# Kernel optimization log

Hardware: AMD Instinct MI355X
Metric: run time of the kernel (lower is better)

Reference implementation:

```python
import jax, jax.numpy as jnp
import numpy as np

COMMITMENT_COST = 0.25

def setup_inputs() -> dict:
    key = jax.random.key(0)
    k1, k2 = jax.random.split(key)
    B, K, D = 32768, 4096, 256
    inputs = jax.random.normal(k1, (B, D), dtype=jnp.float32)
    embedding = jax.random.normal(k2, (K, D), dtype=jnp.float32) * (1.0 / np.sqrt(D))
    return {"inputs": inputs, "embedding": embedding}

def reference(inputs, embedding):
    distances = (
        jnp.sum(inputs * inputs, axis=1, keepdims=True)
        + jnp.sum(embedding * embedding, axis=1)
        - 2.0 * jnp.einsum("bd,kd->bk", inputs, embedding)
    )
    encoding_indices = jnp.argmin(distances, axis=1)  # [B]
    # one-hot @ embedding == gather
    quantized = embedding[encoding_indices]  # [B, D]
    # Eval-mode loss (module in inference mode): q_latent + commitment * e_latent
    e_latent_loss = jnp.mean((inputs - jax.lax.stop_gradient(quantized)) ** 2)
    q_latent_loss = jnp.mean((quantized - jax.lax.stop_gradient(inputs)) ** 2)
    loss = q_latent_loss + COMMITMENT_COST * e_latent_loss
    # Straight-through estimator
    quantized_st = inputs + jax.lax.stop_gradient(quantized - inputs)
    return (quantized_st, loss, encoding_indices)
```

## Files before the change

kernel.cpp:

```cpp
#include <hip/hip_runtime.h>

constexpr int Bsz = 32768;
constexpr int Ksz = 4096;
constexpr int Dsz = 256;

constexpr int KD = 512;
constexpr int NT = 12;
constexpr int NCAND = 16;
constexpr int NFBLK = Bsz / 4;
constexpr float TAU = 1e-3f;

typedef __attribute__((ext_vector_type(8))) short short8;
typedef __attribute__((ext_vector_type(4))) float f32x4;

__device__ __forceinline__ unsigned short f2bf(float f) {
  unsigned u = __float_as_uint(f);
  u += 0x7fffu + ((u >> 16) & 1u);
  return (unsigned short)(u >> 16);
}
__device__ __forceinline__ float bf2f(unsigned short h) {
  return __uint_as_float(((unsigned)h) << 16);
}

__global__ __launch_bounds__(256) void vq_prep_x(const float* __restrict__ X,
                                                 unsigned short* __restrict__ X2) {
  const int tid = blockIdx.x * 256 + threadIdx.x;
  const int row = tid >> 6;
  const int d4 = tid & 63;
  const float4 v = *reinterpret_cast<const float4*>(X + (size_t)row * Dsz + d4 * 4);
  ushort4 h, l;
  h.x = f2bf(v.x); l.x = f2bf(v.x - bf2f(h.x));
  h.y = f2bf(v.y); l.y = f2bf(v.y - bf2f(h.y));
  h.z = f2bf(v.z); l.z = f2bf(v.z - bf2f(h.z));
  h.w = f2bf(v.w); l.w = f2bf(v.w - bf2f(h.w));
  *reinterpret_cast<ushort4*>(X2 + (size_t)row * KD + d4 * 4) = h;
  *reinterpret_cast<ushort4*>(X2 + (size_t)row * KD + 256 + d4 * 4) = l;
}

__global__ __launch_bounds__(256) void vq_prep_e(const float* __restrict__ E,
                                                 unsigned short* __restrict__ E2,
                                                 float* __restrict__ enorm) {
  const int wid = threadIdx.x >> 6;
  const int lane = threadIdx.x & 63;
  const int k = blockIdx.x * 4 + wid;
  const float4 v = *reinterpret_cast<const float4*>(E + (size_t)k * Dsz + lane * 4);
  ushort4 h, l;
  h.x = f2bf(v.x); l.x = f2bf(v.x - bf2f(h.x));
  h.y = f2bf(v.y); l.y = f2bf(v.y - bf2f(h.y));
  h.z = f2bf(v.z); l.z = f2bf(v.z - bf2f(h.z));
  h.w = f2bf(v.w); l.w = f2bf(v.w - bf2f(h.w));
  *reinterpret_cast<ushort4*>(E2 + (size_t)k * KD + lane * 4) = h;
  *reinterpret_cast<ushort4*>(E2 + (size_t)k * KD + 256 + lane * 4) = l;
  float s = v.x * v.x + v.y * v.y + v.z * v.z + v.w * v.w;
#pragma unroll
  for (int off = 32; off > 0; off >>= 1) s += __shfl_down(s, off);
  if (lane == 0) enorm[k] = s;
}

__global__ __launch_bounds__(512, 2) void vq_gemm_argmin(
    const unsigned short* __restrict__ X2, const unsigned short* __restrict__ E2,
    const float* __restrict__ enorm, float4* __restrict__ cand) {
  __shared__ unsigned short sA[2][256 * 64];
  __shared__ unsigned short sB[2][256 * 64];

  const int t5 = threadIdx.x;
  const int lane = t5 & 63;
  const int wid = t5 >> 6;
  const int wm = wid >> 2;
  const int wn = wid & 3;

  const int bid = blockIdx.x;
  const int swz = (bid & 7) * 256 + (bid >> 3);
  const int mb = swz >> 4;
  const int nb = swz & 15;
  const int row0 = mb * 256;
  const int col0 = nb * 256;

  const int srow = lane >> 3;
  const int sslot = (lane & 7) ^ srow;

  const int l15 = lane & 15;
  const int lhi = lane >> 4;
  const int lx = lane & 7;

  f32x4 acc[8][4];
#pragma unroll
  for (int m = 0; m < 8; ++m)
#pragma unroll
    for (int n = 0; n < 4; ++n) acc[m][n] = f32x4{0.f, 0.f, 0.f, 0.f};

#define AOF(kt) ((((kt) >> 2) == 1 ? 256 : 0) + ((kt) & 3) * 64)
#define BOF(kt) ((((kt) >> 2) == 2 ? 256 : 0) + ((kt) & 3) * 64)

#define STAGE(BUFI, AO, BO)                                                    \
  {                                                                            \
    _Pragma("unroll") for (int q = 0; q < 4; ++q) {                            \
      const int r = wid * 32 + q * 8;                                          \
      __builtin_amdgcn_global_load_lds(                                        \
          (const __attribute__((address_space(1))) void*)(                     \
              X2 + (size_t)(row0 + r + srow) * KD + (AO) + sslot * 8),         \
          (__attribute__((address_space(3))) void*)(&sA[BUFI][r * 64]), 16, 0, 0); \
    }                                                                          \
    _Pragma("unroll") for (int q = 0; q < 4; ++q) {                            \
      const int r = wid * 32 + q * 8;                                          \
      __builtin_amdgcn_global_load_lds(                                        \
          (const __attribute__((address_space(1))) void*)(                     \
              E2 + (size_t)(col0 + r + srow) * KD + (BO) + sslot * 8),         \
          (__attribute__((address_space(3))) void*)(&sB[BUFI][r * 64]), 16, 0, 0); \
    }                                                                          \
  }

#define LOADFRAGS(BUFI, KS)                                                    \
  {                                                                            \
    _Pragma("unroll") for (int m = 0; m < 8; ++m)                              \
        af[m] = *reinterpret_cast<const short8*>(                              \
            &sA[BUFI][(wm * 128 + m * 16 + l15) * 64 +                         \
                      (((KS)*4 + lhi) ^ lx) * 8]);                             \
    _Pragma("unroll") for (int n = 0; n < 4; ++n)                              \
        bf[n] = *reinterpret_cast<const short8*>(                              \
            &sB[BUFI][(wn * 64 + n * 16 + l15) * 64 +                          \
                      (((KS)*4 + lhi) ^ lx) * 8]);                             \
  }

#define MFMAS                                                                  \
  {                                                                            \
    _Pragma("unroll") for (int m = 0; m < 8; ++m)                              \
        _Pragma("unroll") for (int n = 0; n < 4; ++n)                          \
            acc[m][n] = __builtin_amdgcn_mfma_f32_16x16x32_bf16(               \
                af[m], bf[n], acc[m][n], 0, 0, 0);                             \
  }

  STAGE(0, AOF(0), BOF(0));
  STAGE(1, AOF(1), BOF(1));

#pragma unroll
  for (int t = 0; t < NT; ++t) {
    const int buf = t & 1;
    short8 af[8], bf[4];

    if (t < NT - 1) {
      asm volatile("s_waitcnt vmcnt(8)" ::: "memory");
    } else {
      asm volatile("s_waitcnt vmcnt(0)" ::: "memory");
    }
    __builtin_amdgcn_sched_barrier(0);
    __builtin_amdgcn_s_barrier();
    __builtin_amdgcn_sched_barrier(0);

    LOADFRAGS(buf, 0);
    asm volatile("s_waitcnt lgkmcnt(0)" ::: "memory");
    __builtin_amdgcn_sched_barrier(0);
    __builtin_amdgcn_s_setprio(1);
    MFMAS;
    __builtin_amdgcn_s_setprio(0);

    LOADFRAGS(buf, 1);
    asm volatile("s_waitcnt lgkmcnt(0)" ::: "memory");
    __builtin_amdgcn_sched_barrier(0);
    __builtin_amdgcn_s_barrier();
    __builtin_amdgcn_sched_barrier(0);

    if (t + 2 < NT) {
      STAGE(buf, AOF(t + 2), BOF(t + 2));
    }
    __builtin_amdgcn_sched_barrier(0);

    __builtin_amdgcn_s_setprio(1);
    MFMAS;
    __builtin_amdgcn_s_setprio(0);
  }

  __syncthreads();

  float en[4];
#pragma unroll
  for (int n = 0; n < 4; ++n) en[n] = enorm[col0 + wn * 64 + n * 16 + l15];

  float4* scr = reinterpret_cast<float4*>(&sA[0][0]);

#pragma unroll
  for (int m = 0; m < 8; ++m) {
#pragma unroll
    for (int q = 0; q < 4; ++q) {
      float v1 = 3.4e38f, v2 = 3.4e38f;
      int ii1 = 0x7fffffff, ii2 = 0x7fffffff;
#pragma unroll
      for (int n = 0; n < 4; ++n) {
        const float s = en[n] - 2.0f * acc[m][n][q];
        const int colg = col0 + wn * 64 + n * 16 + l15;
        if (s < v1) { v2 = v1; ii2 = ii1; v1 = s; ii1 = colg; }
        else if (s < v2) { v2 = s; ii2 = colg; }
      }
#pragma unroll
      for (int mbit = 1; mbit <= 8; mbit <<= 1) {
        const float ov1 = __shfl_xor(v1, mbit);
        const float ov2 = __shfl_xor(v2, mbit);
        const int oi1 = __shfl_xor(ii1, mbit);
        const int oi2 = __shfl_xor(ii2, mbit);
        if (ov1 < v1 || (ov1 == v1 && oi1 < ii1)) {
          float nv2 = v1; int ni2 = ii1;
          if (ov2 < nv2) { nv2 = ov2; ni2 = oi2; }
          v1 = ov1; ii1 = oi1; v2 = nv2; ii2 = ni2;
        } else if (ov1 < v2) {
          v2 = ov1; ii2 = oi1;
        }
      }
      if (l15 == 0) {
        const int rl = wm * 128 + m * 16 + lhi * 4 + q;
        scr[rl * 4 + wn] = make_float4(v1, __int_as_float(ii1),
                                       v2, __int_as_float(ii2));
      }
    }
  }
  __syncthreads();
  if (t5 < 256) {
    float v1 = 3.4e38f, v2 = 3.4e38f;
    int ii1 = 0x7fffffff, ii2 = 0x7fffffff;
#pragma unroll
    for (int j = 0; j < 4; ++j) {
      const float4 c = scr[t5 * 4 + j];
      const float o1 = c.x, o2 = c.z;
      const int a1 = __float_as_int(c.y), a2 = __float_as_int(c.w);
      if (o1 < v1 || (o1 == v1 && a1 < ii1)) {
        float nv2 = v1; int ni2 = ii1;
        if (o2 < nv2) { nv2 = o2; ni2 = a2; }
        v2 = nv2; ii2 = ni2; v1 = o1; ii1 = a1;
      } else if (o1 < v2) {
        v2 = o1; ii2 = a1;
      }
    }
    cand[(size_t)(row0 + t5) * NCAND + nb] =
        make_float4(v1, __int_as_float(ii1), v2, __int_as_float(ii2));
  }
#undef AOF
#undef BOF
#undef STAGE
#undef LOADFRAGS
#undef MFMAS
}

__global__ __launch_bounds__(256) void vq_finalize(
    const float* __restrict__ X, const float* __restrict__ E,
    const float4* __restrict__ cand, float* __restrict__ out,
    float* __restrict__ partial) {
  __shared__ float ls[4];
  const int wid = threadIdx.x >> 6;
  const int lane = threadIdx.x & 63;
  const int b = blockIdx.x * 4 + wid;

  float v1 = 3.4e38f, v2 = 3.4e38f;
  int ii1 = 0x7fffffff, ii2 = 0x7fffffff;
  if (lane < NCAND) {
    const float4 c = cand[(size_t)b * NCAND + lane];
    v1 = c.x; ii1 = __float_as_int(c.y);
    v2 = c.z; ii2 = __float_as_int(c.w);
  }
#pragma unroll
  for (int mbit = 1; mbit <= 8; mbit <<= 1) {
    const float ov1 = __shfl_xor(v1, mbit);
    const float ov2 = __shfl_xor(v2, mbit);
    const int oi1 = __shfl_xor(ii1, mbit);
    const int oi2 = __shfl_xor(ii2, mbit);
    if (ov1 < v1 || (ov1 == v1 && oi1 < ii1)) {
      float nv2 = v1; int ni2 = ii1;
      if (ov2 < nv2) { nv2 = ov2; ni2 = oi2; }
      v1 = ov1; ii1 = oi1; v2 = nv2; ii2 = ni2;
    } else if (ov1 < v2) {
      v2 = ov1; ii2 = oi1;
    }
  }
  v1 = __shfl(v1, 0); v2 = __shfl(v2, 0);
  ii1 = __shfl(ii1, 0); ii2 = __shfl(ii2, 0);

  const float4 x = *reinterpret_cast<const float4*>(X + (size_t)b * Dsz + lane * 4);

  if (v2 - v1 < TAU) {
    const float4 e1 = *reinterpret_cast<const float4*>(E + (size_t)ii1 * Dsz + lane * 4);
    const float4 e2 = *reinterpret_cast<const float4*>(E + (size_t)ii2 * Dsz + lane * 4);
    double d1 = ((double)x.x - e1.x) * ((double)x.x - e1.x) +
                ((double)x.y - e1.y) * ((double)x.y - e1.y) +
                ((double)x.z - e1.z) * ((double)x.z - e1.z) +
                ((double)x.w - e1.w) * ((double)x.w - e1.w);
    double d2 = ((double)x.x - e2.x) * ((double)x.x - e2.x) +
                ((double)x.y - e2.y) * ((double)x.y - e2.y) +
                ((double)x.z - e2.z) * ((double)x.z - e2.z) +
                ((double)x.w - e2.w) * ((double)x.w - e2.w);
#pragma unroll
    for (int mbit = 1; mbit <= 32; mbit <<= 1) {
      d1 += __shfl_xor(d1, mbit);
      d2 += __shfl_xor(d2, mbit);
    }
    if (d2 < d1 || (d2 == d1 && ii2 < ii1)) ii1 = ii2;
  }

  const float4 q = *reinterpret_cast<const float4*>(E + (size_t)ii1 * Dsz + lane * 4);
  *reinterpret_cast<float4*>(out + (size_t)b * Dsz + lane * 4) = q;

  const float dx = x.x - q.x, dy = x.y - q.y, dz = x.z - q.z, dw = x.w - q.w;
  float s2 = dx * dx + dy * dy + dz * dz + dw * dw;
#pragma unroll
  for (int off = 32; off > 0; off >>= 1) s2 += __shfl_down(s2, off);
  if (lane == 0) {
    ls[wid] = s2;
    out[(size_t)Bsz * Dsz + 1 + b] = (float)ii1;
  }
  __syncthreads();
  if (threadIdx.x == 0)
    partial[blockIdx.x] = ls[0] + ls[1] + ls[2] + ls[3];
}

__global__ __launch_bounds__(256) void vq_loss_reduce(const float* __restrict__ partial,
                                                      float* __restrict__ out) {
  __shared__ float ls[4];
  const int wid = threadIdx.x >> 6;
  const int lane = threadIdx.x & 63;
  float s = 0.f;
  for (int i = threadIdx.x; i < NFBLK; i += 256) s += partial[i];
#pragma unroll
  for (int off = 32; off > 0; off >>= 1) s += __shfl_down(s, off);
  if (lane == 0) ls[wid] = s;
  __syncthreads();
  if (threadIdx.x == 0)
    out[(size_t)Bsz * Dsz] = (ls[0] + ls[1] + ls[2] + ls[3]) *
                             (1.25f / ((float)Bsz * (float)Dsz));
}

extern "C" void kernel_launch(void* const* d_in, const int* in_sizes, int n_in,
                              void* d_out, int out_size, void* d_ws, size_t ws_size,
                              hipStream_t stream) {
  const float* X = (const float*)d_in[0];
  const float* E = (const float*)d_in[1];
  float* out = (float*)d_out;

  char* ws = (char*)d_ws;
  float* enorm = (float*)ws;
  unsigned short* X2 = (unsigned short*)(ws + (16 << 10));
  unsigned short* E2 = (unsigned short*)(ws + (16 << 10) + (32 << 20));
  float4* cand = (float4*)(ws + (16 << 10) + (36 << 20));
  float* partial = (float*)(ws + (16 << 10) + (44 << 20));

  vq_prep_x<<<Bsz * 64 / 256, 256, 0, stream>>>(X, X2);
  vq_prep_e<<<Ksz / 4, 256, 0, stream>>>(E, E2, enorm);
  vq_gemm_argmin<<<(Bsz / 256) * (Ksz / 256), 512, 0, stream>>>(X2, E2, enorm, cand);
  vq_finalize<<<NFBLK, 256, 0, stream>>>(X, E, cand, out, partial);
  vq_loss_reduce<<<1, 256, 0, stream>>>(partial, out);
}
```

Measured before the change: 449.4 us.

## Split each K-tile into four quadrant MFMA phases with interleaved LDS fragment loads

Restructures the main GEMM loop so that each tile is processed in four quadrant phases (8 A/B fragments per phase) instead of two full k-step phases. LDS fragment loads for later quadrants happen between MFMA bursts, and the global-load wait is moved to the end of the iteration. The aim is a finer-grained ping-pong schedule that keeps MFMAs busy while LDS reads and global prefetches proceed. In exchange, the kernel executes more s_barrier instructions per tile and a different fragment register layout (af/bf2 indexed by k).

After: 510.4 us. 13.6% more time.

```diff
diff --git a/kernel.cpp b/kernel.cpp
--- a/kernel.cpp
+++ b/kernel.cpp
@@ -110,64 +110,84 @@
     }                                                                          \
   }
 
-#define LOADFRAGS(BUFI, KS)                                                    \
+#define LDA(BUFI, MI, KK, MBASE)                                               \
+  af[(MI)*2 + (KK)] = *reinterpret_cast<const short8*>(                        \
+      &sA[BUFI][(wm * 128 + (MBASE) + (MI)*16 + l15) * 64 +                    \
+                (((KK)*4 + lhi) ^ lx) * 8]);
+#define LDB(BUFI, NI, KK)                                                      \
+  bf2[(NI)*2 + (KK)] = *reinterpret_cast<const short8*>(                       \
+      &sB[BUFI][(wn * 64 + (NI)*16 + l15) * 64 + (((KK)*4 + lhi) ^ lx) * 8]);
+
+#define QMFMA(MB, NB)                                                          \
   {                                                                            \
-    _Pragma("unroll") for (int m = 0; m < 8; ++m)                              \
-        af[m] = *reinterpret_cast<const short8*>(                              \
-            &sA[BUFI][(wm * 128 + m * 16 + l15) * 64 +                         \
-                      (((KS)*4 + lhi) ^ lx) * 8]);                             \
-    _Pragma("unroll") for (int n = 0; n < 4; ++n)                              \
-        bf[n] = *reinterpret_cast<const short8*>(                              \
-            &sB[BUFI][(wn * 64 + n * 16 + l15) * 64 +                          \
-                      (((KS)*4 + lhi) ^ lx) * 8]);                             \
-  }
-
-#define MFMAS                                                                  \
-  {                                                                            \
-    _Pragma("unroll") for (int m = 0; m < 8; ++m)                              \
-        _Pragma("unroll") for (int n = 0; n < 4; ++n)                          \
-            acc[m][n] = __builtin_amdgcn_mfma_f32_16x16x32_bf16(               \
-                af[m], bf[n], acc[m][n], 0, 0, 0);                             \
-  }
+    _Pragma("unroll") for (int kk = 0; kk < 2; ++kk)                           \
+        _Pragma("unroll") for (int mi = 0; mi < 4; ++mi)                       \
+            _Pragma("unroll") for (int ni = 0; ni < 2; ++ni)                   \
+                acc[(MB) + mi][(NB) + ni] =                                    \
+        __builtin_amdgcn_mfma_f32_16x16x32_bf16(                               \
+            af[mi * 2 + kk], bf2[((NB) + ni) * 2 + kk],                        \
+            acc[(MB) + mi][(NB) + ni], 0, 0, 0);                               \
+  }
+
+#define WAITLGKM                                                               \
+  asm volatile("s_waitcnt lgkmcnt(0)" ::: "memory");                           \
+  __builtin_amdgcn_sched_barrier(0);
 
   STAGE(0, AOF(0), BOF(0));
   STAGE(1, AOF(1), BOF(1));
+  asm volatile("s_waitcnt vmcnt(8)" ::: "memory");
+  __builtin_amdgcn_sched_barrier(0);
+  __builtin_amdgcn_s_barrier();
 
 #pragma unroll
   for (int t = 0; t < NT; ++t) {
     const int buf = t & 1;
-    short8 af[8], bf[4];
-
-    if (t < NT - 1) {
-      asm volatile("s_waitcnt vmcnt(8)" ::: "memory");
-    } else {
-      asm volatile("s_waitcnt vmcnt(0)" ::: "memory");
-    }
-    __builtin_amdgcn_sched_barrier(0);
-    __builtin_amdgcn_s_barrier();
-    __builtin_amdgcn_sched_barrier(0);
-
-    LOADFRAGS(buf, 0);
-    asm volatile("s_waitcnt lgkmcnt(0)" ::: "memory");
-    __builtin_amdgcn_sched_barrier(0);
+    short8 af[8], bf2[8];
+
+#pragma unroll
+    for (int mi = 0; mi < 4; ++mi) { LDA(buf, mi, 0, 0); LDA(buf, mi, 1, 0); }
+#pragma unroll
+    for (int ni = 0; ni < 2; ++ni) { LDB(buf, ni, 0); LDB(buf, ni, 1); }
+    __builtin_amdgcn_s_barrier();
+    WAITLGKM;
     __builtin_amdgcn_s_setprio(1);
-    MFMAS;
+    QMFMA(0, 0);
     __builtin_amdgcn_s_setprio(0);
-
-    LOADFRAGS(buf, 1);
-    asm volatile("s_waitcnt lgkmcnt(0)" ::: "memory");
-    __builtin_amdgcn_sched_barrier(0);
-    __builtin_amdgcn_s_barrier();
-    __builtin_amdgcn_sched_barrier(0);
+    __builtin_amdgcn_s_barrier();
+
+#pragma unroll
+    for (int ni = 2; ni < 4; ++ni) { LDB(buf, ni, 0); LDB(buf, ni, 1); }
+    __builtin_amdgcn_s_barrier();
+    WAITLGKM;
+    __builtin_amdgcn_s_setprio(1);
+    QMFMA(0, 2);
+    __builtin_amdgcn_s_setprio(0);
+    __builtin_amdgcn_s_barrier();
+
+#pragma unroll
+    for (int mi = 0; mi < 4; ++mi) { LDA(buf, mi, 0, 64); LDA(buf, mi, 1, 64); }
+    __builtin_amdgcn_s_barrier();
+    WAITLGKM;
+    __builtin_amdgcn_s_setprio(1);
+    QMFMA(4, 0);
+    __builtin_amdgcn_s_setprio(0);
+    __builtin_amdgcn_s_barrier();
 
     if (t + 2 < NT) {
       STAGE(buf, AOF(t + 2), BOF(t + 2));
     }
     __builtin_amdgcn_sched_barrier(0);
-
+    __builtin_amdgcn_s_barrier();
     __builtin_amdgcn_s_setprio(1);
-    MFMAS;
+    QMFMA(4, 2);
     __builtin_amdgcn_s_setprio(0);
+    if (t < NT - 2) {
+      asm volatile("s_waitcnt vmcnt(8)" ::: "memory");
+    } else if (t == NT - 2) {
+      asm volatile("s_waitcnt vmcnt(0)" ::: "memory");
+    }
+    __builtin_amdgcn_sched_barrier(0);
+    __builtin_amdgcn_s_barrier();
   }
 
   __syncthreads();
@@ -235,8 +255,10 @@
 #undef AOF
 #undef BOF
 #undef STAGE
-#undef LOADFRAGS
-#undef MFMAS
+#undef LDA
+#undef LDB
+#undef QMFMA
+#undef WAITLGKM
 }
 
 __global__ __launch_bounds__(256) void vq_finalize(
```
